# Kernel optimization log

Hardware: AMD Instinct MI355X
Metric: run time of the kernel (lower is better)

## Reference

```python
import jax, jax.numpy as jnp
import numpy as np

B, S, H = 4, 2048, 512
I = 1024  # intermediate_dim
E = 8     # num_experts
K = 2     # top_k


def setup_inputs() -> dict:
    key = jax.random.key(0)
    k1, k2, k3, k4 = jax.random.split(key, 4)
    x = jax.random.normal(k1, (B, S, H), dtype=jnp.float32)
    expert_indices = jax.random.randint(k2, (B, S, K), 0, E, dtype=jnp.int32)
    # parameters: init.normal_(std=0.02)
    w13 = 0.02 * jax.random.normal(k3, (E, H, 2 * I), dtype=jnp.float32)
    w2 = 0.02 * jax.random.normal(k4, (E, I, H), dtype=jnp.float32)
    return {"x": x, "expert_indices": expert_indices, "w13": w13, "w2": w2}


def reference(x, expert_indices, w13, w2):
    # x: (B,S,H); expert_indices: (B,S,K); w13: (E,H,2I); w2: (E,I,H)
    # Same math as torch's per-token weight gather + matmul, expressed as
    # dense all-expert GEMM followed by per-token expert selection.
    h13_all = jnp.einsum('bsh,ehd->bsed', x, w13)          # (B,S,E,2I)
    h13 = jnp.take_along_axis(h13_all, expert_indices[..., None], axis=2)  # (B,S,K,2I)
    gate, up = jnp.split(h13, 2, axis=-1)                   # each (B,S,K,I)
    h_inter = jax.nn.silu(gate) * up                        # (B,S,K,I)
    out_all = jnp.einsum('bski,eih->bskeh', h_inter, w2)    # (B,S,K,E,H)
    out = jnp.take_along_axis(out_all, expert_indices[..., None, None], axis=3)
    return out.squeeze(3)                                   # (B,S,K,H)
```

## Files before the change

kernel.cpp:

```cpp
#include <hip/hip_runtime.h>


#define H_DIM 512
#define I_DIM 1024
#define E_NUM 8
#define P_PAIRS 16384
#define CAP P_PAIRS
#define MAX_TILES 136

#define PREP_TW13 2048
#define PREP_TW2 1024
#define PREP_CVT 2048
#define PREP_ROUTE 64
#define PREP_BLOCKS (PREP_TW13 + PREP_TW2 + PREP_CVT + PREP_ROUTE)

typedef _Float16 half8 __attribute__((ext_vector_type(8)));
typedef float f32x4 __attribute__((ext_vector_type(4)));
typedef unsigned int u32;
typedef const __attribute__((address_space(1))) u32* gas_t;
typedef __attribute__((address_space(3))) u32* las_t;

__device__ __forceinline__ void glds16(const void* g, void* l) {
  __builtin_amdgcn_global_load_lds((gas_t)g, (las_t)l, 16, 0, 0);
}

__device__ __forceinline__ bool tile_decode(const int* counts, int ty, int& e,
                                            int& m0, int& ne, int& rb) {
  int base = 0;
  rb = 0;
  for (e = 0; e < E_NUM; ++e) {
    ne = counts[e];
    const int nt = (ne + 127) >> 7;
    if (ty < base + nt) { m0 = (ty - base) << 7; return true; }
    base += nt;
    rb += ne;
  }
  return false;
}

__global__ __launch_bounds__(256) void prep_k(
    const float* __restrict__ x, const int* __restrict__ idx,
    const float* __restrict__ w13, const float* __restrict__ w2,
    int* __restrict__ counts, int* __restrict__ lists,
    _Float16* __restrict__ xh, _Float16* __restrict__ w13t,
    _Float16* __restrict__ w2t) {
  __shared__ __align__(16) _Float16 tile[64][72];
  const int b = blockIdx.x;
  const int tid = threadIdx.x;

  if (b < PREP_TW13 + PREP_TW2) {
    const float* src;
    _Float16* dst;
    int R, C, c0, r0;
    if (b < PREP_TW13) {
      R = H_DIM; C = 2 * I_DIM;
      const int e = b >> 8;
      c0 = (b & 31) * 64;
      r0 = ((b >> 5) & 7) * 64;
      src = w13 + (size_t)e * R * C;
      dst = w13t + (size_t)e * C * R;
    } else {
      const int l = b - PREP_TW13;
      R = I_DIM; C = H_DIM;
      const int e = l >> 7;
      c0 = (l & 7) * 64;
      r0 = ((l >> 3) & 15) * 64;
      src = w2 + (size_t)e * R * C;
      dst = w2t + (size_t)e * C * R;
    }
    {
      const int r = tid >> 4;
      const int c4 = (tid & 15) * 4;
      for (int pass = 0; pass < 4; ++pass) {
        f32x4 v = *(const f32x4*)(src + (size_t)(r0 + pass * 16 + r) * C + c0 + c4);
        for (int j = 0; j < 4; ++j) tile[c4 + j][pass * 16 + r] = (_Float16)v[j];
      }
    }
    __syncthreads();
    {
      const int c = tid >> 3;
      const int r8 = (tid & 7) * 8;
      for (int pass = 0; pass < 2; ++pass) {
        half8 h = *(const half8*)&tile[pass * 32 + c][r8];
        *(half8*)(dst + (size_t)(c0 + pass * 32 + c) * R + r0 + r8) = h;
      }
    }
  } else if (b < PREP_TW13 + PREP_TW2 + PREP_CVT) {
    const int l = b - (PREP_TW13 + PREP_TW2);
    const size_t i = ((size_t)l * 256 + tid) * 8;
    f32x4 v0 = *(const f32x4*)(x + i);
    f32x4 v1 = *(const f32x4*)(x + i + 4);
    half8 h;
    for (int j = 0; j < 4; ++j) { h[j] = (_Float16)v0[j]; h[j + 4] = (_Float16)v1[j]; }
    *(half8*)(xh + i) = h;
  } else {
    int* lcnt = (int*)&tile[0][0];
    int* lbase = lcnt + E_NUM;
    const int l = b - (PREP_TW13 + PREP_TW2 + PREP_CVT);
    if (tid < E_NUM) lcnt[tid] = 0;
    __syncthreads();
    const int p = l * 256 + tid;
    const int e = idx[p];
    const int r = atomicAdd(&lcnt[e], 1);
    __syncthreads();
    if (tid < E_NUM) lbase[tid] = atomicAdd(&counts[tid], lcnt[tid]);
    __syncthreads();
    lists[e * CAP + lbase[e] + r] = p;
  }
}

__global__ __launch_bounds__(256) void gemm1_k(
    const _Float16* __restrict__ xh, const _Float16* __restrict__ w13t,
    const int* __restrict__ counts, const int* __restrict__ lists,
    _Float16* __restrict__ h_ws) {
  int e, m0, ne, rb;
  if (!tile_decode(counts, blockIdx.y, e, m0, ne, rb)) return;
  const int n0 = blockIdx.x * 64;

  __shared__ int rows[128];
  __shared__ __align__(16) _Float16 As[128 * 32];
  __shared__ __align__(16) _Float16 Bgs[64 * 32];
  __shared__ __align__(16) _Float16 Bus[64 * 32];

  const int tid = threadIdx.x;
  if (tid < 128) {
    const int m = m0 + tid;
    rows[tid] = (m < ne) ? lists[e * CAP + m] : -1;
  }
  __syncthreads();

  const int sr = tid >> 2;
  const int s4 = tid & 3;
  const int segoff = ((s4 ^ ((sr >> 1) & 3)) * 8);
  const int pa0 = rows[sr];
  const int pa1 = rows[64 + sr];
  const int t0 = (pa0 >= 0) ? (pa0 >> 1) : 0;
  const int t1 = (pa1 >= 0) ? (pa1 >> 1) : 0;
  const _Float16* ga0 = xh + (size_t)t0 * H_DIM + segoff;
  const _Float16* ga1 = xh + (size_t)t1 * H_DIM + segoff;
  const _Float16* gbg = w13t + ((size_t)e * 2 * I_DIM + n0 + sr) * H_DIM + segoff;
  const _Float16* gbu = gbg + (size_t)I_DIM * H_DIM;
  _Float16* la0 = As + sr * 32 + s4 * 8;
  _Float16* la1 = As + (64 + sr) * 32 + s4 * 8;
  _Float16* lbg = Bgs + sr * 32 + s4 * 8;
  _Float16* lbu = Bus + sr * 32 + s4 * 8;

  const int lane = tid & 63;
  const int wid = tid >> 6;
  const int wm = wid & 1;
  const int wn = wid >> 1;
  const int fm = lane & 15;
  const int q = lane >> 4;
  int aoff[4], boff[2];
  for (int mi = 0; mi < 4; ++mi) {
    const int rA = wm * 64 + mi * 16 + fm;
    aoff[mi] = rA * 32 + ((q ^ ((rA >> 1) & 3)) * 8);
  }
  for (int ni = 0; ni < 2; ++ni) {
    const int cB = wn * 32 + ni * 16 + fm;
    boff[ni] = cB * 32 + ((q ^ ((cB >> 1) & 3)) * 8);
  }

  f32x4 accg[4][2] = {};
  f32x4 accu[4][2] = {};

  for (int k0 = 0; k0 < H_DIM; k0 += 32) {
    glds16(ga0 + k0, la0);
    glds16(ga1 + k0, la1);
    glds16(gbg + k0, lbg);
    glds16(gbu + k0, lbu);
    __syncthreads();

    half8 af[4], bg[2], bu[2];
    for (int mi = 0; mi < 4; ++mi) af[mi] = *(const half8*)&As[aoff[mi]];
    for (int ni = 0; ni < 2; ++ni) {
      bg[ni] = *(const half8*)&Bgs[boff[ni]];
      bu[ni] = *(const half8*)&Bus[boff[ni]];
    }
    for (int mi = 0; mi < 4; ++mi)
      for (int ni = 0; ni < 2; ++ni) {
        accg[mi][ni] = __builtin_amdgcn_mfma_f32_16x16x32_f16(af[mi], bg[ni], accg[mi][ni], 0, 0, 0);
        accu[mi][ni] = __builtin_amdgcn_mfma_f32_16x16x32_f16(af[mi], bu[ni], accu[mi][ni], 0, 0, 0);
      }
    __syncthreads();
  }

  for (int mi = 0; mi < 4; ++mi)
    for (int r = 0; r < 4; ++r) {
      const int mrow = wm * 64 + mi * 16 + q * 4 + r;
      if (m0 + mrow >= ne) continue;
      _Float16* hrow = h_ws + (size_t)(rb + m0 + mrow) * I_DIM + n0;
      for (int ni = 0; ni < 2; ++ni) {
        const int c = wn * 32 + ni * 16 + fm;
        const float g = accg[mi][ni][r];
        const float u = accu[mi][ni][r];
        hrow[c] = (_Float16)(g / (1.0f + __expf(-g)) * u);
      }
    }
}

__global__ __launch_bounds__(256) void gemm2_k(
    const _Float16* __restrict__ h_ws, const _Float16* __restrict__ w2t,
    const int* __restrict__ counts, const int* __restrict__ lists,
    float* __restrict__ out) {
  int e, m0, ne, rb;
  if (!tile_decode(counts, blockIdx.x, e, m0, ne, rb)) return;
  const int n0 = blockIdx.y * 128;

  __shared__ int rows[128];
  __shared__ __align__(16) _Float16 As[128 * 64];
  __shared__ __align__(16) _Float16 Bs[128 * 64];

  const int tid = threadIdx.x;
  if (tid < 128) {
    const int m = m0 + tid;
    rows[tid] = (m < ne) ? lists[e * CAP + m] : -1;
  }

  const int s8 = tid & 7;
  const int sr8 = tid >> 3;
  const int sw = ((s8 ^ (sr8 & 7)) * 8);
  const _Float16* gA[4];
  const _Float16* gB[4];
  _Float16* lA[4];
  _Float16* lB[4];
  for (int pa = 0; pa < 4; ++pa) {
    const int m = pa * 32 + sr8;
    gA[pa] = h_ws + (size_t)(rb + m0 + m) * I_DIM + sw;
    lA[pa] = As + m * 64 + s8 * 8;
    gB[pa] = w2t + ((size_t)e * H_DIM + n0 + m) * I_DIM + sw;
    lB[pa] = Bs + m * 64 + s8 * 8;
  }

  const int lane = tid & 63;
  const int wid = tid >> 6;
  const int wm = wid & 1;
  const int wn = wid >> 1;
  const int fm = lane & 15;
  const int q = lane >> 4;
  int aoff[2][4], boff[2][4];
  for (int ks = 0; ks < 2; ++ks) {
    for (int mi = 0; mi < 4; ++mi) {
      const int rA = wm * 64 + mi * 16 + fm;
      aoff[ks][mi] = rA * 64 + (((ks * 4 + q) ^ (rA & 7)) * 8);
    }
    for (int ni = 0; ni < 4; ++ni) {
      const int cB = wn * 64 + ni * 16 + fm;
      boff[ks][ni] = cB * 64 + (((ks * 4 + q) ^ (cB & 7)) * 8);
    }
  }

  f32x4 acc[4][4] = {};

  for (int k0 = 0; k0 < I_DIM; k0 += 64) {
    for (int pa = 0; pa < 4; ++pa) {
      glds16(gA[pa] + k0, lA[pa]);
      glds16(gB[pa] + k0, lB[pa]);
    }
    __syncthreads();

    for (int ks = 0; ks < 2; ++ks) {
      half8 af[4], bf[4];
      for (int mi = 0; mi < 4; ++mi) af[mi] = *(const half8*)&As[aoff[ks][mi]];
      for (int ni = 0; ni < 4; ++ni) bf[ni] = *(const half8*)&Bs[boff[ks][ni]];
      for (int mi = 0; mi < 4; ++mi)
        for (int ni = 0; ni < 4; ++ni)
          acc[mi][ni] = __builtin_amdgcn_mfma_f32_16x16x32_f16(af[mi], bf[ni], acc[mi][ni], 0, 0, 0);
    }
    __syncthreads();
  }

  for (int mi = 0; mi < 4; ++mi)
    for (int r = 0; r < 4; ++r) {
      const int mrow = wm * 64 + mi * 16 + q * 4 + r;
      const int p = rows[mrow];
      if (p < 0) continue;
      float* orow = out + (size_t)p * H_DIM + n0;
      for (int ni = 0; ni < 4; ++ni)
        orow[wn * 64 + ni * 16 + fm] = acc[mi][ni][r];
    }
}

extern "C" void kernel_launch(void* const* d_in, const int* in_sizes, int n_in,
                              void* d_out, int out_size, void* d_ws, size_t ws_size,
                              hipStream_t stream) {
  const float* x = (const float*)d_in[0];
  const int* idx = (const int*)d_in[1];
  const float* w13 = (const float*)d_in[2];
  const float* w2 = (const float*)d_in[3];

  char* ws = (char*)d_ws;
  int* counts = (int*)ws;
  int* lists = (int*)(ws + 2048);
  const size_t OFF_XH = 2048 + (size_t)E_NUM * CAP * 4;
  const size_t OFF_W13T = OFF_XH + (size_t)P_PAIRS / 2 * H_DIM * 2;
  const size_t OFF_W2T = OFF_W13T + (size_t)E_NUM * 2 * I_DIM * H_DIM * 2;
  const size_t OFF_H = OFF_W2T + (size_t)E_NUM * H_DIM * I_DIM * 2;
  _Float16* xh = (_Float16*)(ws + OFF_XH);
  _Float16* w13t = (_Float16*)(ws + OFF_W13T);
  _Float16* w2t = (_Float16*)(ws + OFF_W2T);
  _Float16* h_ws = (_Float16*)(ws + OFF_H);

  hipMemsetAsync(d_ws, 0, 128, stream);
  prep_k<<<dim3(PREP_BLOCKS), 256, 0, stream>>>(x, idx, w13, w2, counts, lists,
                                                xh, w13t, w2t);
  gemm1_k<<<dim3(I_DIM / 64, MAX_TILES), 256, 0, stream>>>(
      xh, w13t, counts, lists, h_ws);
  gemm2_k<<<dim3(MAX_TILES, H_DIM / 128), 256, 0, stream>>>(
      h_ws, w2t, counts, lists, (float*)d_out);
}
```

Baseline: 201.8 us.

## Double-buffer LDS in both expert GEMMs and halve gemm2 N-tile

```diff
diff --git a/kernel.cpp b/kernel.cpp
--- a/kernel.cpp
+++ b/kernel.cpp
@@ -118,9 +118,9 @@
   const int n0 = blockIdx.x * 64;
 
   __shared__ int rows[128];
-  __shared__ __align__(16) _Float16 As[128 * 32];
-  __shared__ __align__(16) _Float16 Bgs[64 * 32];
-  __shared__ __align__(16) _Float16 Bus[64 * 32];
+  __shared__ __align__(16) _Float16 As[2][128 * 32];
+  __shared__ __align__(16) _Float16 Bgs[2][64 * 32];
+  __shared__ __align__(16) _Float16 Bus[2][64 * 32];
 
   const int tid = threadIdx.x;
   if (tid < 128) {
@@ -140,10 +140,9 @@
   const _Float16* ga1 = xh + (size_t)t1 * H_DIM + segoff;
   const _Float16* gbg = w13t + ((size_t)e * 2 * I_DIM + n0 + sr) * H_DIM + segoff;
   const _Float16* gbu = gbg + (size_t)I_DIM * H_DIM;
-  _Float16* la0 = As + sr * 32 + s4 * 8;
-  _Float16* la1 = As + (64 + sr) * 32 + s4 * 8;
-  _Float16* lbg = Bgs + sr * 32 + s4 * 8;
-  _Float16* lbu = Bus + sr * 32 + s4 * 8;
+  const int la0 = sr * 32 + s4 * 8;
+  const int la1 = (64 + sr) * 32 + s4 * 8;
+  const int lb = sr * 32 + s4 * 8;
 
   const int lane = tid & 63;
   const int wid = tid >> 6;
@@ -164,26 +163,43 @@
   f32x4 accg[4][2] = {};
   f32x4 accu[4][2] = {};
 
-  for (int k0 = 0; k0 < H_DIM; k0 += 32) {
-    glds16(ga0 + k0, la0);
-    glds16(ga1 + k0, la1);
-    glds16(gbg + k0, lbg);
-    glds16(gbu + k0, lbu);
-    __syncthreads();
-
-    half8 af[4], bg[2], bu[2];
-    for (int mi = 0; mi < 4; ++mi) af[mi] = *(const half8*)&As[aoff[mi]];
-    for (int ni = 0; ni < 2; ++ni) {
-      bg[ni] = *(const half8*)&Bgs[boff[ni]];
-      bu[ni] = *(const half8*)&Bus[boff[ni]];
-    }
-    for (int mi = 0; mi < 4; ++mi)
-      for (int ni = 0; ni < 2; ++ni) {
-        accg[mi][ni] = __builtin_amdgcn_mfma_f32_16x16x32_f16(af[mi], bg[ni], accg[mi][ni], 0, 0, 0);
-        accu[mi][ni] = __builtin_amdgcn_mfma_f32_16x16x32_f16(af[mi], bu[ni], accu[mi][ni], 0, 0, 0);
-      }
-    __syncthreads();
-  }
+#define G1_STAGE(buf, k0)                    \
+  do {                                       \
+    glds16(ga0 + (k0), &As[buf][la0]);       \
+    glds16(ga1 + (k0), &As[buf][la1]);       \
+    glds16(gbg + (k0), &Bgs[buf][lb]);       \
+    glds16(gbu + (k0), &Bus[buf][lb]);       \
+  } while (0)
+
+#define G1_COMPUTE(buf)                                                         \
+  do {                                                                          \
+    half8 af[4], bg[2], bu[2];                                                  \
+    for (int mi = 0; mi < 4; ++mi) af[mi] = *(const half8*)&As[buf][aoff[mi]];  \
+    for (int ni = 0; ni < 2; ++ni) {                                            \
+      bg[ni] = *(const half8*)&Bgs[buf][boff[ni]];                              \
+      bu[ni] = *(const half8*)&Bus[buf][boff[ni]];                              \
+    }                                                                           \
+    for (int mi = 0; mi < 4; ++mi)                                              \
+      for (int ni = 0; ni < 2; ++ni) {                                          \
+        accg[mi][ni] = __builtin_amdgcn_mfma_f32_16x16x32_f16(                  \
+            af[mi], bg[ni], accg[mi][ni], 0, 0, 0);                             \
+        accu[mi][ni] = __builtin_amdgcn_mfma_f32_16x16x32_f16(                  \
+            af[mi], bu[ni], accu[mi][ni], 0, 0, 0);                             \
+      }                                                                         \
+  } while (0)
+
+  G1_STAGE(0, 0);
+  __syncthreads();
+  for (int k0 = 0; k0 < H_DIM; k0 += 64) {
+    G1_STAGE(1, k0 + 32);
+    G1_COMPUTE(0);
+    __syncthreads();
+    if (k0 + 64 < H_DIM) G1_STAGE(0, k0 + 64);
+    G1_COMPUTE(1);
+    __syncthreads();
+  }
+#undef G1_STAGE
+#undef G1_COMPUTE
 
   for (int mi = 0; mi < 4; ++mi)
     for (int r = 0; r < 4; ++r) {
@@ -205,11 +221,11 @@
     float* __restrict__ out) {
   int e, m0, ne, rb;
   if (!tile_decode(counts, blockIdx.x, e, m0, ne, rb)) return;
-  const int n0 = blockIdx.y * 128;
+  const int n0 = blockIdx.y * 64;
 
   __shared__ int rows[128];
-  __shared__ __align__(16) _Float16 As[128 * 64];
-  __shared__ __align__(16) _Float16 Bs[128 * 64];
+  __shared__ __align__(16) _Float16 As[2][128 * 64];
+  __shared__ __align__(16) _Float16 Bs[2][64 * 64];
 
   const int tid = threadIdx.x;
   if (tid < 128) {
@@ -221,15 +237,20 @@
   const int sr8 = tid >> 3;
   const int sw = ((s8 ^ (sr8 & 7)) * 8);
   const _Float16* gA[4];
-  const _Float16* gB[4];
-  _Float16* lA[4];
-  _Float16* lB[4];
+  int lA[4];
   for (int pa = 0; pa < 4; ++pa) {
     const int m = pa * 32 + sr8;
-    gA[pa] = h_ws + (size_t)(rb + m0 + m) * I_DIM + sw;
-    lA[pa] = As + m * 64 + s8 * 8;
-    gB[pa] = w2t + ((size_t)e * H_DIM + n0 + m) * I_DIM + sw;
-    lB[pa] = Bs + m * 64 + s8 * 8;
+    int grow = rb + m0 + m;
+    if (grow > P_PAIRS - 1) grow = P_PAIRS - 1;
+    gA[pa] = h_ws + (size_t)grow * I_DIM + sw;
+    lA[pa] = m * 64 + s8 * 8;
+  }
+  const _Float16* gB[2];
+  int lB[2];
+  for (int pb = 0; pb < 2; ++pb) {
+    const int n = pb * 32 + sr8;
+    gB[pb] = w2t + ((size_t)e * H_DIM + n0 + n) * I_DIM + sw;
+    lB[pb] = n * 64 + s8 * 8;
   }
 
   const int lane = tid & 63;
@@ -238,37 +259,55 @@
   const int wn = wid >> 1;
   const int fm = lane & 15;
   const int q = lane >> 4;
-  int aoff[2][4], boff[2][4];
+  int aoff[2][4], boff[2][2];
   for (int ks = 0; ks < 2; ++ks) {
     for (int mi = 0; mi < 4; ++mi) {
       const int rA = wm * 64 + mi * 16 + fm;
       aoff[ks][mi] = rA * 64 + (((ks * 4 + q) ^ (rA & 7)) * 8);
     }
-    for (int ni = 0; ni < 4; ++ni) {
-      const int cB = wn * 64 + ni * 16 + fm;
+    for (int ni = 0; ni < 2; ++ni) {
+      const int cB = wn * 32 + ni * 16 + fm;
       boff[ks][ni] = cB * 64 + (((ks * 4 + q) ^ (cB & 7)) * 8);
     }
   }
 
-  f32x4 acc[4][4] = {};
-
-  for (int k0 = 0; k0 < I_DIM; k0 += 64) {
-    for (int pa = 0; pa < 4; ++pa) {
-      glds16(gA[pa] + k0, lA[pa]);
-      glds16(gB[pa] + k0, lB[pa]);
-    }
-    __syncthreads();
-
-    for (int ks = 0; ks < 2; ++ks) {
-      half8 af[4], bf[4];
-      for (int mi = 0; mi < 4; ++mi) af[mi] = *(const half8*)&As[aoff[ks][mi]];
-      for (int ni = 0; ni < 4; ++ni) bf[ni] = *(const half8*)&Bs[boff[ks][ni]];
-      for (int mi = 0; mi < 4; ++mi)
-        for (int ni = 0; ni < 4; ++ni)
-          acc[mi][ni] = __builtin_amdgcn_mfma_f32_16x16x32_f16(af[mi], bf[ni], acc[mi][ni], 0, 0, 0);
-    }
-    __syncthreads();
-  }
+  f32x4 acc[4][2] = {};
+
+#define G2_STAGE(buf, k0)                                  \
+  do {                                                     \
+    for (int pa = 0; pa < 4; ++pa)                         \
+      glds16(gA[pa] + (k0), &As[buf][lA[pa]]);             \
+    for (int pb = 0; pb < 2; ++pb)                         \
+      glds16(gB[pb] + (k0), &Bs[buf][lB[pb]]);             \
+  } while (0)
+
+#define G2_COMPUTE(buf)                                                          \
+  do {                                                                           \
+    for (int ks = 0; ks < 2; ++ks) {                                             \
+      half8 af[4], bf[2];                                                        \
+      for (int mi = 0; mi < 4; ++mi)                                             \
+        af[mi] = *(const half8*)&As[buf][aoff[ks][mi]];                          \
+      for (int ni = 0; ni < 2; ++ni)                                             \
+        bf[ni] = *(const half8*)&Bs[buf][boff[ks][ni]];                          \
+      for (int mi = 0; mi < 4; ++mi)                                             \
+        for (int ni = 0; ni < 2; ++ni)                                           \
+          acc[mi][ni] = __builtin_amdgcn_mfma_f32_16x16x32_f16(                  \
+              af[mi], bf[ni], acc[mi][ni], 0, 0, 0);                             \
+    }                                                                            \
+  } while (0)
+
+  G2_STAGE(0, 0);
+  __syncthreads();
+  for (int k0 = 0; k0 < I_DIM; k0 += 128) {
+    G2_STAGE(1, k0 + 64);
+    G2_COMPUTE(0);
+    __syncthreads();
+    if (k0 + 128 < I_DIM) G2_STAGE(0, k0 + 128);
+    G2_COMPUTE(1);
+    __syncthreads();
+  }
+#undef G2_STAGE
+#undef G2_COMPUTE
 
   for (int mi = 0; mi < 4; ++mi)
     for (int r = 0; r < 4; ++r) {
@@ -276,8 +315,8 @@
       const int p = rows[mrow];
       if (p < 0) continue;
       float* orow = out + (size_t)p * H_DIM + n0;
-      for (int ni = 0; ni < 4; ++ni)
-        orow[wn * 64 + ni * 16 + fm] = acc[mi][ni][r];
+      for (int ni = 0; ni < 2; ++ni)
+        orow[wn * 32 + ni * 16 + fm] = acc[mi][ni][r];
     }
 }
 
@@ -306,6 +345,6 @@
                                                 xh, w13t, w2t);
   gemm1_k<<<dim3(I_DIM / 64, MAX_TILES), 256, 0, stream>>>(
       xh, w13t, counts, lists, h_ws);
-  gemm2_k<<<dim3(MAX_TILES, H_DIM / 128), 256, 0, stream>>>(
+  gemm2_k<<<dim3(MAX_TILES, H_DIM / 64), 256, 0, stream>>>(
       h_ws, w2t, counts, lists, (float*)d_out);
 }
```

New measurement: 206.6 us. 2.4% more time.
